# Kernel tuning notes

Hardware: AMD Instinct MI355X
Metric: run time of the kernel (lower is better)

## Reference

```python
import jax, jax.numpy as jnp
import numpy as np

N = 131072
E = 524288
H = 128
EPS = 1e-5

def _layernorm(h, g, b):
    mu = jnp.mean(h, axis=-1, keepdims=True)
    var = jnp.mean((h - mu) ** 2, axis=-1, keepdims=True)
    return (h - mu) * jax.lax.rsqrt(var + EPS) * g + b

def _node_to_node(x, senders, receivers, valid, num_nodes, params):
    # two-way (symmetrized) message passing: gather + scatter_add, then MLP+LN
    W1, b1, W2, b2, W3, b3, g, beta = params
    tws = jnp.concatenate([senders, receivers])
    twr = jnp.concatenate([receivers, senders])
    msg = x[tws]  # [2E', H] gather
    if valid is not None:
        msg = jnp.where(jnp.concatenate([valid, valid])[:, None], msg, 0.0)
    agg = jax.ops.segment_sum(msg, twr, num_segments=num_nodes)  # scatter_add
    h = jax.nn.gelu(agg @ W1 + b1, approximate=False)
    h = jax.nn.gelu(h @ W2 + b2, approximate=False)
    h = h @ W3 + b3
    return _layernorm(h, g, beta)

def setup_inputs() -> dict:
    key = jax.random.key(0)
    ks = jax.random.split(key, 20)
    s = 0.05
    inp = {
        "x": jax.random.normal(ks[0], (N, H), dtype=jnp.float32),
        "edge_index": jax.random.randint(ks[1], (2, E), 0, N, dtype=jnp.int32),
        "pool_p": jax.random.normal(ks[2], (H,), dtype=jnp.float32),
    }
    names = ["dW1", "db1", "dW2", "db2", "dW3", "db3", "dg", "dbeta",
             "uW1", "ub1", "uW2", "ub2", "uW3", "ub3", "ug", "ubeta"]
    shapes = [(H, H), (H,), (H, H), (H,), (H, H), (H,), (H,), (H,),
              (2 * H, H), (H,), (H, H), (H,), (H, H), (H,), (H,), (H,)]
    for i, (nm, sh) in enumerate(zip(names, shapes)):
        if nm in ("dg", "ug"):
            inp[nm] = jnp.ones(sh, dtype=jnp.float32)
        elif nm in ("dbeta", "ubeta") or nm.startswith(("db", "ub")):
            inp[nm] = jnp.zeros(sh, dtype=jnp.float32)
        else:
            inp[nm] = jax.random.normal(ks[3 + i], sh, dtype=jnp.float32) * s
    return inp

def reference(x, edge_index, pool_p,
              dW1, db1, dW2, db2, dW3, db3, dg, dbeta,
              uW1, ub1, uW2, ub2, uW3, ub3, ug, ubeta):
    senders, receivers = edge_index[0], edge_index[1]
    k = N // 2  # TopKPooling ratio=0.5

    # ---- down: TopKPooling ----
    score = x @ pool_p / jnp.linalg.norm(pool_p)  # [N]
    _, perm = jax.lax.top_k(score, k)             # kept node indices
    x_skip = x
    x_p = x[perm] * jnp.tanh(score[perm])[:, None]  # [k, H]
    mask = jnp.zeros((N,), dtype=bool).at[perm].set(True)
    mapping = jnp.zeros((N,), dtype=jnp.int32).at[perm].set(
        jnp.arange(k, dtype=jnp.int32))
    valid = mask[senders] & mask[receivers]
    ps, pr = mapping[senders], mapping[receivers]

    # down conv on pooled graph
    x_d = _node_to_node(x_p, ps, pr, valid, k,
                        (dW1, db1, dW2, db2, dW3, db3, dg, dbeta))

    # ---- up: unpool (indexed scatter write) + skip concat + up conv ----
    recovered = jnp.zeros_like(x_skip).at[perm].set(x_d)
    x_u = jnp.concatenate([recovered, x_skip], axis=-1)  # [N, 2H]
    out = _node_to_node(x_u, senders, receivers, None, N,
                        (uW1, ub1, uW2, ub2, uW3, ub3, ug, ubeta))
    return out
```

## Files before the change

kernel.cpp:

```cpp
#include <hip/hip_runtime.h>

#define N_NODES 131072
#define N_EDGES 524288
#define K_TOP   65536
#define LN_EPS  1e-5f
#define N_TILES (N_NODES / 64)

typedef unsigned int u32;
typedef unsigned short u16;
typedef unsigned long long u64;

typedef __attribute__((ext_vector_type(8))) short bf8;
typedef __attribute__((ext_vector_type(4))) float f4;

#define ST_OFF    0
#define CANON_OFF (64u<<10)
#define PART_OFF  (576u<<10)
#define KEYS_OFF  (1u<<20)
#define TVAL_OFF  (2u<<20)
#define KEPT_OFF  ((2u<<20)+(512u<<10))
#define SBUF_OFF  (3u<<20)
#define OFF_OFF   (35u<<20)
#define ADJ_OFF   (36u<<20)


#define C_DW1 0
#define C_DB1 16384
#define C_DW2 16512
#define C_DB2 32896
#define C_DW3 33024
#define C_DB3 49408
#define C_DG  49536
#define C_DBE 49664
#define C_UW1 49792
#define C_UB1 82560
#define C_UW2 82688
#define C_UB2 99072
#define C_UW3 99200
#define C_UB3 115584
#define C_UG  115712
#define C_UBE 115840
#define C_TOT 115968
#define CT_DW1 115968
#define CT_DW2 132352
#define CT_DW3 148736
#define CT_UW1 165120
#define CT_UW2 197888
#define CT_UW3 214272
#define CT_TOT 230656
#define T_REGION (CT_TOT - CT_DW1)

__device__ __forceinline__ float bflo(u32 u){ return __uint_as_float(u << 16); }
__device__ __forceinline__ float bfhi(u32 u){ return __uint_as_float(u & 0xFFFF0000u); }
__device__ __forceinline__ float bf2f(u16 v){ return __uint_as_float(((u32)v) << 16); }
__device__ __forceinline__ u32 f2bf(float f){
  u32 u = __float_as_uint(f);
  return (u + 0x7FFFu + ((u >> 16) & 1u)) >> 16;
}
__device__ __forceinline__ float gelu_f(float x){
  return 0.5f * x * (1.0f + erff(x * 0.7071067811865476f));
}

__device__ __forceinline__ int swz16(int row, int cc){
  return row * 128 + ((cc ^ (row & 15)) * 8);
}

__device__ __forceinline__ bf8 ld_bf16_chunk(const u32* __restrict__ rowp, int s, int quad){
  uint4 v = *(const uint4*)(rowp + s * 16 + quad * 4);
  return __builtin_bit_cast(bf8, v);
}
__device__ __forceinline__ bf8 scale_bf16_chunk(const u32* __restrict__ rowp, int s, int quad, float tv){
  uint4 v = *(const uint4*)(rowp + s * 16 + quad * 4);
  uint4 q;
  q.x = f2bf(bflo(v.x) * tv) | (f2bf(bfhi(v.x) * tv) << 16);
  q.y = f2bf(bflo(v.y) * tv) | (f2bf(bfhi(v.y) * tv) << 16);
  q.z = f2bf(bflo(v.z) * tv) | (f2bf(bfhi(v.z) * tv) << 16);
  q.w = f2bf(bflo(v.w) * tv) | (f2bf(bfhi(v.w) * tv) << 16);
  return __builtin_bit_cast(bf8, q);
}
__device__ __forceinline__ bf8 cvt_f32_chunk(const float* __restrict__ rowp, int s, int quad, float tv){
  const float* p = rowp + s * 32 + quad * 8;
  float4 f0 = *(const float4*)p;
  float4 f1 = *(const float4*)(p + 4);
  uint4 q;
  q.x = f2bf(f0.x * tv) | (f2bf(f0.y * tv) << 16);
  q.y = f2bf(f0.z * tv) | (f2bf(f0.w * tv) << 16);
  q.z = f2bf(f1.x * tv) | (f2bf(f1.y * tv) << 16);
  q.w = f2bf(f1.z * tv) | (f2bf(f1.w * tv) << 16);
  return __builtin_bit_cast(bf8, q);
}

__device__ __forceinline__ void gemm_ab(const u16* ws, const bf8 a[4], int mn, int quad, f4 acc[8]){
  #pragma unroll
  for (int s = 0; s < 4; s++){
    #pragma unroll
    for (int j = 0; j < 8; j++){
      bf8 b = *(const bf8*)&ws[swz16(j * 16 + mn, s * 4 + quad)];
      acc[j] = __builtin_amdgcn_mfma_f32_16x16x32_bf16(a[s], b, acc[j], 0, 0, 0);
    }
  }
}

struct SelState {
  u64 prefix;
  u32 krem, eqcnt;
  int is_f32;
  u32 pad;
  double inv_norm;
  u32 eqlist[4096];
  u64 eqkey[4096];
};

struct P16 { const void* q[16]; };

__global__ void k_detect(const u32* __restrict__ xw, SelState* st){
  int t = threadIdx.x;
  int cnt = 0;
  for (int i = t; i < 4096; i += 256){
    u32 w = xw[(size_t)i * 2048];
    u32 e = (w >> 23) & 0xFFu;
    if (e >= 97u && e <= 135u) cnt++;
  }
  __shared__ int sh[256];
  sh[t] = cnt; __syncthreads();
  for (int o = 128; o > 0; o >>= 1){ if (t < o) sh[t] += sh[t+o]; __syncthreads(); }
  if (t == 0) st->is_f32 = (sh[0] >= 3072) ? 1 : 0;
}

__global__ void k_init(SelState* st){
  if (threadIdx.x == 0){ st->prefix = 0; st->krem = K_TOP; st->eqcnt = 0; }
}

__global__ void k_canon(P16 ps, const SelState* __restrict__ st, u16* __restrict__ canon){
  const int off[17] = {C_DW1,C_DB1,C_DW2,C_DB2,C_DW3,C_DB3,C_DG,C_DBE,
                       C_UW1,C_UB1,C_UW2,C_UB2,C_UW3,C_UB3,C_UG,C_UBE,C_TOT};
  int i = blockIdx.x * 256 + threadIdx.x;
  if (i >= C_TOT) return;
  int seg = 0;
  #pragma unroll
  for (int s2 = 0; s2 < 16; s2++) if (i >= off[s2+1]) seg = s2 + 1;
  int j = i - off[seg];
  if (st->is_f32) canon[i] = (u16)f2bf(((const float*)ps.q[seg])[j]);
  else            canon[i] = ((const u16*)ps.q[seg])[j];
}

__global__ void k_canon_t(u16* __restrict__ canon){
  const int src[6] = {C_DW1, C_DW2, C_DW3, C_UW1, C_UW2, C_UW3};
  const int dst[7] = {CT_DW1, CT_DW2, CT_DW3, CT_UW1, CT_UW2, CT_UW3, CT_TOT};
  int i = blockIdx.x * 256 + threadIdx.x;
  if (i >= T_REGION) return;
  int g = CT_DW1 + i;
  int seg = 0;
  #pragma unroll
  for (int s2 = 0; s2 < 6; s2++) if (g >= dst[s2+1]) seg = s2 + 1;
  int loc = g - dst[seg];
  int K = (seg == 3) ? 256 : 128;
  int n = loc / K, k = loc % K;
  canon[g] = canon[src[seg] + k * 128 + n];
}

__global__ void k_pnorm(const void* __restrict__ p, SelState* st){
  int t = threadIdx.x;
  float pv = st->is_f32 ? ((const float*)p)[t] : bf2f(((const u16*)p)[t]);
  __shared__ double sh[128];
  sh[t] = (double)pv * (double)pv;
  __syncthreads();
  for (int o = 64; o > 0; o >>= 1){ if (t < o) sh[t] += sh[t+o]; __syncthreads(); }
  if (t == 0) st->inv_norm = 1.0 / sqrt(sh[0]);
}

__global__ __launch_bounds__(256) void k_score(const void* __restrict__ xraw, const void* __restrict__ praw,
                        const SelState* __restrict__ st,
                        u64* __restrict__ keys, float* __restrict__ tval){
  int t = threadIdx.x, lane = t & 63, w = t >> 6;
  int n = blockIdx.x * 4 + w;
  double d;
  if (st->is_f32){
    const float* xf = (const float*)xraw + (size_t)n * 128;
    const float* pf = (const float*)praw;
    d = (double)xf[lane] * (double)pf[lane]
      + (double)xf[64 + lane] * (double)pf[64 + lane];
  } else {
    const u32* xw = (const u32*)xraw + (size_t)n * 64;
    const u32* pw = (const u32*)praw;
    u32 xx = xw[lane], pv = pw[lane];
    d = (double)bflo(xx) * (double)bflo(pv) + (double)bfhi(xx) * (double)bfhi(pv);
  }
  for (int o = 32; o > 0; o >>= 1) d += __shfl_down(d, o, 64);
  if (lane == 0){
    double sc = d * st->inv_norm;
    u64 u = (u64)__double_as_longlong(sc);
    u64 key = (u & 0x8000000000000000ULL) ? ~u : (u | 0x8000000000000000ULL);
    keys[n] = key;
    tval[n] = tanhf((float)sc);
  }
}

__global__ __launch_bounds__(256) void k_histp(const u64* __restrict__ keys,
                                               const SelState* __restrict__ st,
                                               u32* __restrict__ partial, int pass){
  __shared__ u32 h[256];
  int t = threadIdx.x;
  h[t] = 0;
  __syncthreads();
  u64 pref = st->prefix;
  int sh_d = 56 - 8 * pass;
  for (int n = blockIdx.x * 256 + t; n < N_NODES; n += 256 * 256){
    u64 k = keys[n];
    bool m = (pass == 0) ? true : ((k >> (sh_d + 8)) == pref);
    if (m) atomicAdd(&h[(u32)((k >> sh_d) & 255)], 1u);
  }
  __syncthreads();
  partial[blockIdx.x * 256 + t] = h[t];
}

__global__ void k_scanp(const u32* __restrict__ partial, SelState* st){
  __shared__ u32 tot[256];
  int t = threadIdx.x;
  u32 s = 0;
  for (int b = 0; b < 256; b++) s += partial[b * 256 + t];
  tot[t] = s;
  __syncthreads();
  if (t == 0){
    u32 target = st->krem;
    u32 cum = 0; int chosen = 255;
    for (int b = 255; b >= 0; b--){
      if (cum + tot[b] >= target){ chosen = b; break; }
      cum += tot[b];
    }
    st->prefix = (st->prefix << 8) | (u64)(u32)chosen;
    st->krem = target - cum;
  }
}

__global__ void k_mark(const u64* __restrict__ keys, SelState* st, u32* __restrict__ kept){
  int n = blockIdx.x * blockDim.x + threadIdx.x;
  u64 k = keys[n];
  u32 t32 = (u32)(k >> 32);
  u32 T = (u32)st->prefix;
  kept[n] = (t32 > T) ? 1u : 0u;
  if (t32 == T){
    u32 i = atomicAdd(&st->eqcnt, 1u);
    if (i < 4096){ st->eqlist[i] = (u32)n; st->eqkey[i] = k; }
  }
}

__global__ void k_tie(SelState* st, u32* __restrict__ kept){
  u32 m = st->eqcnt; if (m > 4096) m = 4096;
  u32 r = st->krem;
  for (u32 i = threadIdx.x; i < m; i += blockDim.x){
    u64 ki = st->eqkey[i]; u32 ii = st->eqlist[i];
    u32 rank = 0;
    for (u32 j = 0; j < m; j++){
      u64 kj = st->eqkey[j];
      rank += (kj > ki || (kj == ki && st->eqlist[j] < ii)) ? 1u : 0u;
    }
    if (rank < r) kept[ii] = 1u;
  }
}

__global__ __launch_bounds__(256) void k_deg(const int* __restrict__ se, const int* __restrict__ re,
                                             u32* __restrict__ deg){
  int e = blockIdx.x * 256 + threadIdx.x;
  int s = se[e], r = re[e];
  atomicAdd(&deg[s], 1u);
  atomicAdd(&deg[r], 1u);
}

__global__ __launch_bounds__(256) void k_scan1(const u32* __restrict__ deg, u32* __restrict__ bsum){
  __shared__ u32 sh[256];
  int t = threadIdx.x;
  int base = blockIdx.x * 1024 + t * 4;
  u32 s = deg[base] + deg[base+1] + deg[base+2] + deg[base+3];
  sh[t] = s; __syncthreads();
  for (int o = 128; o > 0; o >>= 1){ if (t < o) sh[t] += sh[t+o]; __syncthreads(); }
  if (t == 0) bsum[blockIdx.x] = sh[0];
}

__global__ void k_scan2(u32* __restrict__ bsum){
  __shared__ u32 sh[128];
  int t = threadIdx.x;
  u32 v = bsum[t];
  sh[t] = v; __syncthreads();
  for (int o = 1; o < 128; o <<= 1){
    u32 x = (t >= o) ? sh[t-o] : 0u;
    __syncthreads();
    sh[t] += x;
    __syncthreads();
  }
  bsum[t] = sh[t] - v;
}

__global__ __launch_bounds__(256) void k_scan3(const u32* __restrict__ bsum,
                                               const u32* __restrict__ deg, u32* __restrict__ off){
  __shared__ u32 sh[256];
  int t = threadIdx.x;
  int base = blockIdx.x * 1024 + t * 4;
  u32 v0 = deg[base], v1 = deg[base+1], v2 = deg[base+2], v3 = deg[base+3];
  u32 s = v0 + v1 + v2 + v3;
  sh[t] = s; __syncthreads();
  for (int o = 1; o < 256; o <<= 1){
    u32 x = (t >= o) ? sh[t-o] : 0u;
    __syncthreads();
    sh[t] += x;
    __syncthreads();
  }
  u32 ex = sh[t] - s + bsum[blockIdx.x];
  off[base]   = ex; ex += v0;
  off[base+1] = ex; ex += v1;
  off[base+2] = ex; ex += v2;
  off[base+3] = ex;
  if (blockIdx.x == 0 && t == 0) off[N_NODES] = 2u * N_EDGES;
}

__global__ void k_gcinit(const u32* __restrict__ off, u32* __restrict__ gcur){
  int t = threadIdx.x;
  gcur[t] = off[t * 512];
}

__global__ __launch_bounds__(256) void k_bin(const int* __restrict__ se, const int* __restrict__ re,
                                             u32* __restrict__ gcur, u32* __restrict__ pairs){
  __shared__ u32 cnt[256], sc[256], base[256], cur[256], gpos[256];
  __shared__ u32 stage[8192];
  int t = threadIdx.x;
  cnt[t] = 0;
  __syncthreads();
  int e0 = blockIdx.x * 4096;
  for (int i = t; i < 4096; i += 256){
    int s = se[e0 + i], r = re[e0 + i];
    atomicAdd(&cnt[(u32)r >> 9], 1u);
    atomicAdd(&cnt[(u32)s >> 9], 1u);
  }
  __syncthreads();
  sc[t] = cnt[t];
  __syncthreads();
  for (int o = 1; o < 256; o <<= 1){
    u32 x = (t >= o) ? sc[t - o] : 0u;
    __syncthreads();
    sc[t] += x;
    __syncthreads();
  }
  base[t] = sc[t] - cnt[t];
  cur[t] = base[t];
  gpos[t] = atomicAdd(&gcur[t], cnt[t]);
  __syncthreads();
  for (int i = t; i < 4096; i += 256){
    u32 s = (u32)se[e0 + i], r = (u32)re[e0 + i];
    u32 b1 = r >> 9, p1 = ((r & 511u) << 17) | s;
    u32 b2 = s >> 9, p2 = ((s & 511u) << 17) | r;
    stage[atomicAdd(&cur[b1], 1u)] = p1;
    stage[atomicAdd(&cur[b2], 1u)] = p2;
  }
  __syncthreads();
  int lane = t & 63, wv = t >> 6;
  for (int b = wv; b < 256; b += 4){
    u32 n = cnt[b], src = base[b], dst = gpos[b];
    for (u32 i = lane; i < n; i += 64)
      pairs[dst + i] = stage[src + i];
  }
}

__global__ __launch_bounds__(256) void k_place(const u32* __restrict__ off,
                                               const u32* __restrict__ pairs,
                                               u32* __restrict__ adj){
  __shared__ u32 offl[513];
  __shared__ u32 curl[512];
  int b = blockIdx.x, t = threadIdx.x;
  for (int i = t; i < 513; i += 256) offl[i] = off[b * 512 + i];
  for (int i = t; i < 512; i += 256) curl[i] = 0;
  __syncthreads();
  u32 beg = offl[0], end = offl[512];
  for (u32 i = beg + t; i < end; i += 256){
    u32 p = pairs[i];
    u32 nl = p >> 17, m = p & 0x1FFFFu;
    u32 slot = offl[nl] + atomicAdd(&curl[nl], 1u);
    adj[slot] = m;
  }
}


__global__ __launch_bounds__(256, 3) void k_proj_down(
    const void* __restrict__ xraw, const float* __restrict__ tval,
    const u16* __restrict__ W1T, const SelState* __restrict__ st,
    const u32* __restrict__ kept, u32* __restrict__ S)
{
  __shared__ u16 w1s[128 * 128];
  __shared__ u16 os[64 * 128];
  int t = threadIdx.x, lane = t & 63, wv = t >> 6;
  int m0 = wv * 16, mn = lane & 15, quad = lane >> 4;

  for (int i = t; i < 2048; i += 256){
    int row = i >> 4, cc = i & 15;
    *(uint4*)&w1s[swz16(row, cc)] = *(const uint4*)(W1T + row * 128 + cc * 8);
  }
  int isf = st->is_f32;
  __syncthreads();

  for (int tile = blockIdx.x; tile < N_TILES; tile += gridDim.x){
    int row0 = tile * 64;
    int arow = row0 + m0 + mn;
    float tv = tval[arow];
    bf8 a[4];
    if (isf){
      const float* xf = (const float*)xraw + (size_t)arow * 128;
      #pragma unroll
      for (int s = 0; s < 4; s++) a[s] = cvt_f32_chunk(xf, s, quad, tv);
    } else {
      const u32* xw = (const u32*)xraw + (size_t)arow * 64;
      #pragma unroll
      for (int s = 0; s < 4; s++) a[s] = scale_bf16_chunk(xw, s, quad, tv);
    }
    f4 acc[8];
    #pragma unroll
    for (int j = 0; j < 8; j++){ acc[j][0]=0.f; acc[j][1]=0.f; acc[j][2]=0.f; acc[j][3]=0.f; }
    gemm_ab(w1s, a, mn, quad, acc);

    #pragma unroll
    for (int j = 0; j < 8; j++){
      int c = j * 16 + mn;
      #pragma unroll
      for (int rg = 0; rg < 4; rg++){
        int row = m0 + quad * 4 + rg;
        os[row * 128 + ((c >> 3) ^ (row & 15)) * 8 + (c & 7)] = (u16)f2bf(acc[j][rg]);
      }
    }
    __builtin_amdgcn_wave_barrier();
    int rl = m0 + (lane >> 2), qt = lane & 3;
    u32 kp = kept[row0 + rl];
    u32* out = S + (size_t)(row0 + rl) * 64;
    #pragma unroll
    for (int i = 0; i < 4; i++){
      int cc = qt * 4 + i;
      uint4 w = *(const uint4*)&os[swz16(rl, cc)];
      if (!kp){ w.x = 0; w.y = 0; w.z = 0; w.w = 0; }
      *(uint4*)(out + cc * 4) = w;
    }
    __builtin_amdgcn_wave_barrier();
  }
}

__global__ __launch_bounds__(256, 2) void k_proj_up(
    const u32* __restrict__ R, const void* __restrict__ xraw,
    const u16* __restrict__ W1T, const SelState* __restrict__ st,
    u32* __restrict__ S2)
{
  __shared__ u16 was[128 * 128];
  __shared__ u16 wbs[128 * 128];
  __shared__ u16 os[64 * 128];
  int t = threadIdx.x, lane = t & 63, wv = t >> 6;
  int m0 = wv * 16, mn = lane & 15, quad = lane >> 4;

  for (int i = t; i < 2048; i += 256){
    int row = i >> 4, cc = i & 15;
    *(uint4*)&was[swz16(row, cc)] = *(const uint4*)(W1T + row * 256 + cc * 8);
    *(uint4*)&wbs[swz16(row, cc)] = *(const uint4*)(W1T + row * 256 + 128 + cc * 8);
  }
  int isf = st->is_f32;
  __syncthreads();

  for (int tile = blockIdx.x; tile < N_TILES; tile += gridDim.x){
    int row0 = tile * 64;
    int arow = row0 + m0 + mn;
    bf8 a[4];
    const u32* rp = R + (size_t)arow * 64;
    #pragma unroll
    for (int s = 0; s < 4; s++) a[s] = ld_bf16_chunk(rp, s, quad);
    f4 acc[8];
    #pragma unroll
    for (int j = 0; j < 8; j++){ acc[j][0]=0.f; acc[j][1]=0.f; acc[j][2]=0.f; acc[j][3]=0.f; }
    gemm_ab(was, a, mn, quad, acc);

    if (isf){
      const float* xf = (const float*)xraw + (size_t)arow * 128;
      #pragma unroll
      for (int s = 0; s < 4; s++) a[s] = cvt_f32_chunk(xf, s, quad, 1.0f);
    } else {
      const u32* xw = (const u32*)xraw + (size_t)arow * 64;
      #pragma unroll
      for (int s = 0; s < 4; s++) a[s] = ld_bf16_chunk(xw, s, quad);
    }
    gemm_ab(wbs, a, mn, quad, acc);

    #pragma unroll
    for (int j = 0; j < 8; j++){
      int c = j * 16 + mn;
      #pragma unroll
      for (int rg = 0; rg < 4; rg++){
        int row = m0 + quad * 4 + rg;
        os[row * 128 + ((c >> 3) ^ (row & 15)) * 8 + (c & 7)] = (u16)f2bf(acc[j][rg]);
      }
    }
    __builtin_amdgcn_wave_barrier();
    int rl = m0 + (lane >> 2), qt = lane & 3;
    u32* out = S2 + (size_t)(row0 + rl) * 64;
    #pragma unroll
    for (int i = 0; i < 4; i++){
      int cc = qt * 4 + i;
      *(uint4*)(out + cc * 4) = *(const uint4*)&os[swz16(rl, cc)];
    }
    __builtin_amdgcn_wave_barrier();
  }
}

template<int IS_DOWN>
__global__ __launch_bounds__(256, 4) void k_agg(
    const u32* __restrict__ Smsg, const u32* __restrict__ off, const u32* __restrict__ adj,
    const u16* __restrict__ cb1, const u32* __restrict__ kept,
    u32* __restrict__ H)
{
  int t = threadIdx.x, lane = t & 63, wv = t >> 6;
  float b1l = bf2f(cb1[2 * lane]), b1h = bf2f(cb1[2 * lane + 1]);
  int base = blockIdx.x * 16 + wv * 4;
  #pragma unroll 1
  for (int rr = 0; rr < 4; rr++){
    int n = base + rr;
    if (IS_DOWN && !kept[n]){ H[(size_t)n * 64 + lane] = 0u; continue; }
    u32 jb = off[n], je = off[n + 1];
    float a0 = 0.f, a1 = 0.f;
    u32 j = jb;
    for (; j + 8 <= je; j += 8){
      u32 e0 = adj[j],   e1 = adj[j+1], e2 = adj[j+2], e3 = adj[j+3];
      u32 e4 = adj[j+4], e5 = adj[j+5], e6 = adj[j+6], e7 = adj[j+7];
      u32 w0 = Smsg[(size_t)e0 * 64 + lane];
      u32 w1 = Smsg[(size_t)e1 * 64 + lane];
      u32 w2 = Smsg[(size_t)e2 * 64 + lane];
      u32 w3 = Smsg[(size_t)e3 * 64 + lane];
      u32 w4 = Smsg[(size_t)e4 * 64 + lane];
      u32 w5 = Smsg[(size_t)e5 * 64 + lane];
      u32 w6 = Smsg[(size_t)e6 * 64 + lane];
      u32 w7 = Smsg[(size_t)e7 * 64 + lane];
      a0 += ((bflo(w0) + bflo(w1)) + (bflo(w2) + bflo(w3)))
          + ((bflo(w4) + bflo(w5)) + (bflo(w6) + bflo(w7)));
      a1 += ((bfhi(w0) + bfhi(w1)) + (bfhi(w2) + bfhi(w3)))
          + ((bfhi(w4) + bfhi(w5)) + (bfhi(w6) + bfhi(w7)));
    }
    for (; j + 4 <= je; j += 4){
      u32 e0 = adj[j], e1 = adj[j+1], e2 = adj[j+2], e3 = adj[j+3];
      u32 w0 = Smsg[(size_t)e0 * 64 + lane];
      u32 w1 = Smsg[(size_t)e1 * 64 + lane];
      u32 w2 = Smsg[(size_t)e2 * 64 + lane];
      u32 w3 = Smsg[(size_t)e3 * 64 + lane];
      a0 += (bflo(w0) + bflo(w1)) + (bflo(w2) + bflo(w3));
      a1 += (bfhi(w0) + bfhi(w1)) + (bfhi(w2) + bfhi(w3));
    }
    for (; j < je; j++){
      u32 w = Smsg[(size_t)adj[j] * 64 + lane];
      a0 += bflo(w); a1 += bfhi(w);
    }
    H[(size_t)n * 64 + lane] = f2bf(gelu_f(a0 + b1l)) | (f2bf(gelu_f(a1 + b1h)) << 16);
  }
}

template<int IS_DOWN>
__global__ __launch_bounds__(256, 2) void k_mlp(
    const u32* __restrict__ H,
    const u16* __restrict__ cW2T, const u16* __restrict__ cb2,
    const u16* __restrict__ cW3T, const u16* __restrict__ cb3,
    const u16* __restrict__ cg, const u16* __restrict__ cbe,
    const u32* __restrict__ kept, const SelState* __restrict__ st,
    u32* __restrict__ Rout, void* __restrict__ fout)
{
  __shared__ u16 w2s[128 * 128];
  __shared__ u16 w3s[128 * 128];
  __shared__ u16 os[64 * 128];
  int t = threadIdx.x, lane = t & 63, wv = t >> 6;
  int m0 = wv * 16, mn = lane & 15, quad = lane >> 4;

  for (int i = t; i < 2048; i += 256){
    int row = i >> 4, cc = i & 15;
    *(uint4*)&w2s[swz16(row, cc)] = *(const uint4*)(cW2T + row * 128 + cc * 8);
    *(uint4*)&w3s[swz16(row, cc)] = *(const uint4*)(cW3T + row * 128 + cc * 8);
  }
  float b2v[8], b3v[8], gv[8], bev[8];
  #pragma unroll
  for (int j = 0; j < 8; j++){
    int c = j * 16 + mn;
    b2v[j] = bf2f(cb2[c]); b3v[j] = bf2f(cb3[c]);
    gv[j]  = bf2f(cg[c]);  bev[j] = bf2f(cbe[c]);
  }
  int isf = st->is_f32;
  __syncthreads();

  for (int tile = blockIdx.x; tile < N_TILES; tile += gridDim.x){
    int row0 = tile * 64;
    int arow = row0 + m0 + mn;

    bf8 a[4];
    const u32* hp = H + (size_t)arow * 64;
    #pragma unroll
    for (int s = 0; s < 4; s++) a[s] = ld_bf16_chunk(hp, s, quad);
    f4 acc[8];
    #pragma unroll
    for (int j = 0; j < 8; j++){ acc[j][0]=0.f; acc[j][1]=0.f; acc[j][2]=0.f; acc[j][3]=0.f; }
    gemm_ab(w2s, a, mn, quad, acc);

    #pragma unroll
    for (int j = 0; j < 8; j++){
      int c = j * 16 + mn;
      #pragma unroll
      for (int rg = 0; rg < 4; rg++){
        int row = m0 + quad * 4 + rg;
        os[row * 128 + ((c >> 3) ^ (row & 15)) * 8 + (c & 7)] = (u16)f2bf(gelu_f(acc[j][rg] + b2v[j]));
      }
    }
    __builtin_amdgcn_wave_barrier();

    #pragma unroll
    for (int s = 0; s < 4; s++) a[s] = *(const bf8*)&os[swz16(m0 + mn, s * 4 + quad)];
    #pragma unroll
    for (int j = 0; j < 8; j++){ acc[j][0]=0.f; acc[j][1]=0.f; acc[j][2]=0.f; acc[j][3]=0.f; }
    gemm_ab(w3s, a, mn, quad, acc);

    #pragma unroll
    for (int j = 0; j < 8; j++){
      #pragma unroll
      for (int rg = 0; rg < 4; rg++) acc[j][rg] += b3v[j];
    }
    float s1[4] = {0.f,0.f,0.f,0.f}, s2[4] = {0.f,0.f,0.f,0.f};
    #pragma unroll
    for (int j = 0; j < 8; j++){
      #pragma unroll
      for (int rg = 0; rg < 4; rg++){
        float v = acc[j][rg];
        s1[rg] += v; s2[rg] += v * v;
      }
    }
    #pragma unroll
    for (int o = 1; o < 16; o <<= 1){
      #pragma unroll
      for (int rg = 0; rg < 4; rg++){
        s1[rg] += __shfl_xor(s1[rg], o, 64);
        s2[rg] += __shfl_xor(s2[rg], o, 64);
      }
    }
    float mu[4], rs[4];
    #pragma unroll
    for (int rg = 0; rg < 4; rg++){
      mu[rg] = s1[rg] * 0.0078125f;
      float var = s2[rg] * 0.0078125f - mu[rg] * mu[rg];
      rs[rg] = rsqrtf(var + LN_EPS);
    }
    #pragma unroll
    for (int j = 0; j < 8; j++){
      #pragma unroll
      for (int rg = 0; rg < 4; rg++)
        acc[j][rg] = (acc[j][rg] - mu[rg]) * rs[rg] * gv[j] + bev[j];
    }

    if (!IS_DOWN && isf){
      float* fo = (float*)fout;
      #pragma unroll
      for (int j = 0; j < 8; j++){
        #pragma unroll
        for (int rg = 0; rg < 4; rg++)
          fo[(size_t)(row0 + m0 + quad * 4 + rg) * 128 + j * 16 + mn] = acc[j][rg];
      }
      continue;
    }

    __builtin_amdgcn_wave_barrier();
    #pragma unroll
    for (int j = 0; j < 8; j++){
      int c = j * 16 + mn;
      #pragma unroll
      for (int rg = 0; rg < 4; rg++){
        int row = m0 + quad * 4 + rg;
        os[row * 128 + ((c >> 3) ^ (row & 15)) * 8 + (c & 7)] = (u16)f2bf(acc[j][rg]);
      }
    }
    __builtin_amdgcn_wave_barrier();
    int rl = m0 + (lane >> 2), qt = lane & 3;
    u32 kp = IS_DOWN ? kept[row0 + rl] : 1u;
    u32* out = (IS_DOWN ? Rout : (u32*)fout) + (size_t)(row0 + rl) * 64;
    #pragma unroll
    for (int i = 0; i < 4; i++){
      int cc = qt * 4 + i;
      uint4 w = *(const uint4*)&os[swz16(rl, cc)];
      if (!kp){ w.x = 0; w.y = 0; w.z = 0; w.w = 0; }
      *(uint4*)(out + cc * 4) = w;
    }
    __builtin_amdgcn_wave_barrier();
  }
}


extern "C" void kernel_launch(void* const* d_in, const int* in_sizes, int n_in,
                              void* d_out, int out_size, void* d_ws, size_t ws_size,
                              hipStream_t stream)
{
  const void* x     = d_in[0];
  const int* eidx   = (const int*)d_in[1];
  const void* poolp = d_in[2];
  const int* senders = eidx;
  const int* receivers = eidx + N_EDGES;

  char* ws = (char*)d_ws;
  SelState* st = (SelState*)(ws + ST_OFF);
  u16*  canon  = (u16*) (ws + CANON_OFF);
  u32*  partial= (u32*) (ws + PART_OFF);
  u64*  keys   = (u64*) (ws + KEYS_OFF);
  float* tval  = (float*)(ws + TVAL_OFF);
  u32*  kept   = (u32*) (ws + KEPT_OFF);
  u32*  Sbuf   = (u32*) (ws + SBUF_OFF);
  u32*  off    = (u32*) (ws + OFF_OFF);
  u32*  adj    = (u32*) (ws + ADJ_OFF);
  u32*  deg    = (u32*) (ws + KEYS_OFF);
  u32*  bsum   = partial;
  u32*  gcur   = partial + 512;
  u32*  pairs  = Sbuf;
  u32*  Dbuf   = (u32*) d_out;

  P16 ps;
  for (int i = 0; i < 16; i++) ps.q[i] = d_in[3 + i];

  k_detect<<<1, 256, 0, stream>>>((const u32*)x, st);
  k_init<<<1, 64, 0, stream>>>(st);
  k_canon<<<(C_TOT + 255) / 256, 256, 0, stream>>>(ps, st, canon);
  k_canon_t<<<(T_REGION + 255) / 256, 256, 0, stream>>>(canon);
  k_pnorm<<<1, 128, 0, stream>>>(poolp, st);
  k_score<<<N_NODES / 4, 256, 0, stream>>>(x, poolp, st, keys, tval);
  for (int pass = 0; pass < 4; pass++){
    k_histp<<<256, 256, 0, stream>>>(keys, st, partial, pass);
    k_scanp<<<1, 256, 0, stream>>>(partial, st);
  }
  k_mark<<<N_NODES / 256, 256, 0, stream>>>(keys, st, kept);
  k_tie<<<1, 256, 0, stream>>>(st, kept);

  hipMemsetAsync(deg, 0, (size_t)N_NODES * 4, stream);
  k_deg<<<N_EDGES / 256, 256, 0, stream>>>(senders, receivers, deg);
  k_scan1<<<128, 256, 0, stream>>>(deg, bsum);
  k_scan2<<<1, 128, 0, stream>>>(bsum);
  k_scan3<<<128, 256, 0, stream>>>(bsum, deg, off);
  k_gcinit<<<1, 256, 0, stream>>>(off, gcur);
  k_bin<<<N_EDGES / 4096, 256, 0, stream>>>(senders, receivers, gcur, pairs);
  k_place<<<256, 256, 0, stream>>>(off, pairs, adj);

  k_proj_down<<<768, 256, 0, stream>>>(x, tval, canon + CT_DW1, st, kept, Sbuf);
  k_agg<1><<<N_NODES / 16, 256, 0, stream>>>(Sbuf, off, adj, canon + C_DB1, kept, Dbuf);
  k_mlp<1><<<512, 256, 0, stream>>>(Dbuf,
      canon + CT_DW2, canon + C_DB2, canon + CT_DW3, canon + C_DB3,
      canon + C_DG, canon + C_DBE, kept, st, Sbuf, nullptr);

  k_proj_up<<<512, 256, 0, stream>>>(Sbuf, x, canon + CT_UW1, st, Dbuf);
  k_agg<0><<<N_NODES / 16, 256, 0, stream>>>(Dbuf, off, adj, canon + C_UB1, kept, Sbuf);
  k_mlp<0><<<512, 256, 0, stream>>>(Sbuf,
      canon + CT_UW2, canon + C_UB2, canon + CT_UW3, canon + C_UB3,
      canon + C_UG, canon + C_UBE, kept, st, nullptr, d_out);
}
```

Before: 525.1 us.

## Merge small setup kernels and mask dropped senders in down aggregation

Folds state init into k_detect, merges the weight canonicalization and transpose kernels into one, and computes the pool-vector norm inside k_score. It also zeroes degrees in k_mark instead of a memset, and initializes gcur and a zero row inside k_scan3. These changes cut about five kernel launches and a memset. In the down aggregation, messages from non-kept senders are redirected to a zero row, which adds a per-edge kept lookup. This may be a correctness fix if the projected buffer holds garbage for dropped nodes.

```diff
diff --git a/kernel.cpp b/kernel.cpp
--- a/kernel.cpp
+++ b/kernel.cpp
@@ -20,6 +20,7 @@
 #define TVAL_OFF  (2u<<20)
 #define KEPT_OFF  ((2u<<20)+(512u<<10))
 #define SBUF_OFF  (3u<<20)
+#define DEG_OFF   (34u<<20)
 #define OFF_OFF   (35u<<20)
 #define ADJ_OFF   (36u<<20)
 
@@ -48,7 +49,6 @@
 #define CT_UW2 197888
 #define CT_UW3 214272
 #define CT_TOT 230656
-#define T_REGION (CT_TOT - CT_DW1)
 
 __device__ __forceinline__ float bflo(u32 u){ return __uint_as_float(u << 16); }
 __device__ __forceinline__ float bfhi(u32 u){ return __uint_as_float(u & 0xFFFF0000u); }
@@ -59,6 +59,9 @@
 }
 __device__ __forceinline__ float gelu_f(float x){
   return 0.5f * x * (1.0f + erff(x * 0.7071067811865476f));
+}
+__device__ __forceinline__ float2 f2add(float2 a, float2 b){
+  return make_float2(a.x + b.x, a.y + b.y);
 }
 
 __device__ __forceinline__ int swz16(int row, int cc){
@@ -124,49 +127,39 @@
   __shared__ int sh[256];
   sh[t] = cnt; __syncthreads();
   for (int o = 128; o > 0; o >>= 1){ if (t < o) sh[t] += sh[t+o]; __syncthreads(); }
-  if (t == 0) st->is_f32 = (sh[0] >= 3072) ? 1 : 0;
-}
-
-__global__ void k_init(SelState* st){
-  if (threadIdx.x == 0){ st->prefix = 0; st->krem = K_TOP; st->eqcnt = 0; }
+  if (t == 0){
+    st->is_f32 = (sh[0] >= 3072) ? 1 : 0;
+    st->prefix = 0; st->krem = K_TOP; st->eqcnt = 0;
+  }
 }
 
 __global__ void k_canon(P16 ps, const SelState* __restrict__ st, u16* __restrict__ canon){
-  const int off[17] = {C_DW1,C_DB1,C_DW2,C_DB2,C_DW3,C_DB3,C_DG,C_DBE,
-                       C_UW1,C_UB1,C_UW2,C_UB2,C_UW3,C_UB3,C_UG,C_UBE,C_TOT};
   int i = blockIdx.x * 256 + threadIdx.x;
-  if (i >= C_TOT) return;
-  int seg = 0;
-  #pragma unroll
-  for (int s2 = 0; s2 < 16; s2++) if (i >= off[s2+1]) seg = s2 + 1;
-  int j = i - off[seg];
-  if (st->is_f32) canon[i] = (u16)f2bf(((const float*)ps.q[seg])[j]);
-  else            canon[i] = ((const u16*)ps.q[seg])[j];
-}
-
-__global__ void k_canon_t(u16* __restrict__ canon){
-  const int src[6] = {C_DW1, C_DW2, C_DW3, C_UW1, C_UW2, C_UW3};
-  const int dst[7] = {CT_DW1, CT_DW2, CT_DW3, CT_UW1, CT_UW2, CT_UW3, CT_TOT};
-  int i = blockIdx.x * 256 + threadIdx.x;
-  if (i >= T_REGION) return;
-  int g = CT_DW1 + i;
-  int seg = 0;
-  #pragma unroll
-  for (int s2 = 0; s2 < 6; s2++) if (g >= dst[s2+1]) seg = s2 + 1;
-  int loc = g - dst[seg];
-  int K = (seg == 3) ? 256 : 128;
-  int n = loc / K, k = loc % K;
-  canon[g] = canon[src[seg] + k * 128 + n];
-}
-
-__global__ void k_pnorm(const void* __restrict__ p, SelState* st){
-  int t = threadIdx.x;
-  float pv = st->is_f32 ? ((const float*)p)[t] : bf2f(((const u16*)p)[t]);
-  __shared__ double sh[128];
-  sh[t] = (double)pv * (double)pv;
-  __syncthreads();
-  for (int o = 64; o > 0; o >>= 1){ if (t < o) sh[t] += sh[t+o]; __syncthreads(); }
-  if (t == 0) st->inv_norm = 1.0 / sqrt(sh[0]);
+  if (i >= CT_TOT) return;
+  int isf = st->is_f32;
+  if (i < C_TOT){
+    const int off[17] = {C_DW1,C_DB1,C_DW2,C_DB2,C_DW3,C_DB3,C_DG,C_DBE,
+                         C_UW1,C_UB1,C_UW2,C_UB2,C_UW3,C_UB3,C_UG,C_UBE,C_TOT};
+    int seg = 0;
+    #pragma unroll
+    for (int s2 = 0; s2 < 16; s2++) if (i >= off[s2+1]) seg = s2 + 1;
+    int j = i - off[seg];
+    if (isf) canon[i] = (u16)f2bf(((const float*)ps.q[seg])[j]);
+    else     canon[i] = ((const u16*)ps.q[seg])[j];
+  } else {
+    const int dst[7] = {CT_DW1, CT_DW2, CT_DW3, CT_UW1, CT_UW2, CT_UW3, CT_TOT};
+    const int wq[6]  = {0, 2, 4, 8, 10, 12};
+    int g = i;
+    int seg = 0;
+    #pragma unroll
+    for (int s2 = 0; s2 < 6; s2++) if (g >= dst[s2+1]) seg = s2 + 1;
+    int loc = g - dst[seg];
+    int K = (seg == 3) ? 256 : 128;
+    int n = loc / K, k = loc % K;
+    int src = k * 128 + n;
+    if (isf) canon[g] = (u16)f2bf(((const float*)ps.q[wq[seg]])[src]);
+    else     canon[g] = ((const u16*)ps.q[wq[seg]])[src];
+  }
 }
 
 __global__ __launch_bounds__(256) void k_score(const void* __restrict__ xraw, const void* __restrict__ praw,
@@ -174,21 +167,27 @@
                         u64* __restrict__ keys, float* __restrict__ tval){
   int t = threadIdx.x, lane = t & 63, w = t >> 6;
   int n = blockIdx.x * 4 + w;
-  double d;
+  double d, ps;
   if (st->is_f32){
     const float* xf = (const float*)xraw + (size_t)n * 128;
     const float* pf = (const float*)praw;
-    d = (double)xf[lane] * (double)pf[lane]
-      + (double)xf[64 + lane] * (double)pf[64 + lane];
+    double p0 = (double)pf[lane], p1 = (double)pf[64 + lane];
+    d  = (double)xf[lane] * p0 + (double)xf[64 + lane] * p1;
+    ps = p0 * p0 + p1 * p1;
   } else {
     const u32* xw = (const u32*)xraw + (size_t)n * 64;
     const u32* pw = (const u32*)praw;
     u32 xx = xw[lane], pv = pw[lane];
-    d = (double)bflo(xx) * (double)bflo(pv) + (double)bfhi(xx) * (double)bfhi(pv);
-  }
-  for (int o = 32; o > 0; o >>= 1) d += __shfl_down(d, o, 64);
+    double p0 = (double)bflo(pv), p1 = (double)bfhi(pv);
+    d  = (double)bflo(xx) * p0 + (double)bfhi(xx) * p1;
+    ps = p0 * p0 + p1 * p1;
+  }
+  for (int o = 32; o > 0; o >>= 1){
+    d  += __shfl_down(d,  o, 64);
+    ps += __shfl_down(ps, o, 64);
+  }
   if (lane == 0){
-    double sc = d * st->inv_norm;
+    double sc = d * (1.0 / sqrt(ps));
     u64 u = (u64)__double_as_longlong(sc);
     u64 key = (u & 0x8000000000000000ULL) ? ~u : (u | 0x8000000000000000ULL);
     keys[n] = key;
@@ -233,12 +232,14 @@
   }
 }
 
-__global__ void k_mark(const u64* __restrict__ keys, SelState* st, u32* __restrict__ kept){
+__global__ void k_mark(const u64* __restrict__ keys, SelState* st, u32* __restrict__ kept,
+                       u32* __restrict__ deg){
   int n = blockIdx.x * blockDim.x + threadIdx.x;
   u64 k = keys[n];
   u32 t32 = (u32)(k >> 32);
   u32 T = (u32)st->prefix;
   kept[n] = (t32 > T) ? 1u : 0u;
+  deg[n] = 0u;
   if (t32 == T){
     u32 i = atomicAdd(&st->eqcnt, 1u);
     if (i < 4096){ st->eqlist[i] = (u32)n; st->eqkey[i] = k; }
@@ -292,7 +293,8 @@
 }
 
 __global__ __launch_bounds__(256) void k_scan3(const u32* __restrict__ bsum,
-                                               const u32* __restrict__ deg, u32* __restrict__ off){
+                                               const u32* __restrict__ deg, u32* __restrict__ off,
+                                               u32* __restrict__ gcur, u32* __restrict__ zrow){
   __shared__ u32 sh[256];
   int t = threadIdx.x;
   int base = blockIdx.x * 1024 + t * 4;
@@ -306,16 +308,15 @@
     __syncthreads();
   }
   u32 ex = sh[t] - s + bsum[blockIdx.x];
+  if ((t & 127) == 0) gcur[base >> 9] = ex;
   off[base]   = ex; ex += v0;
   off[base+1] = ex; ex += v1;
   off[base+2] = ex; ex += v2;
   off[base+3] = ex;
-  if (blockIdx.x == 0 && t == 0) off[N_NODES] = 2u * N_EDGES;
-}
-
-__global__ void k_gcinit(const u32* __restrict__ off, u32* __restrict__ gcur){
-  int t = threadIdx.x;
-  gcur[t] = off[t * 512];
+  if (blockIdx.x == 0){
+    if (t == 0) off[N_NODES] = 2u * N_EDGES;
+    if (t < 64) zrow[t] = 0u;
+  }
 }
 
 __global__ __launch_bounds__(256) void k_bin(const int* __restrict__ se, const int* __restrict__ re,
@@ -503,10 +504,19 @@
 }
 
 template<int IS_DOWN>
+__device__ __forceinline__ const u32* rowsel(const u32* __restrict__ Smsg, u32 e,
+                                             const u32* __restrict__ kept,
+                                             const u32* __restrict__ zrow){
+  const u32* p = Smsg + (size_t)e * 64;
+  if (IS_DOWN) p = kept[e] ? p : zrow;
+  return p;
+}
+
+template<int IS_DOWN>
 __global__ __launch_bounds__(256, 4) void k_agg(
     const u32* __restrict__ Smsg, const u32* __restrict__ off, const u32* __restrict__ adj,
     const u16* __restrict__ cb1, const u32* __restrict__ kept,
-    u32* __restrict__ H)
+    const u32* __restrict__ zrow, u32* __restrict__ H)
 {
   int t = threadIdx.x, lane = t & 63, wv = t >> 6;
   float b1l = bf2f(cb1[2 * lane]), b1h = bf2f(cb1[2 * lane + 1]);
@@ -516,38 +526,48 @@
     int n = base + rr;
     if (IS_DOWN && !kept[n]){ H[(size_t)n * 64 + lane] = 0u; continue; }
     u32 jb = off[n], je = off[n + 1];
-    float a0 = 0.f, a1 = 0.f;
+    float2 a = make_float2(0.f, 0.f);
     u32 j = jb;
     for (; j + 8 <= je; j += 8){
-      u32 e0 = adj[j],   e1 = adj[j+1], e2 = adj[j+2], e3 = adj[j+3];
-      u32 e4 = adj[j+4], e5 = adj[j+5], e6 = adj[j+6], e7 = adj[j+7];
-      u32 w0 = Smsg[(size_t)e0 * 64 + lane];
-      u32 w1 = Smsg[(size_t)e1 * 64 + lane];
-      u32 w2 = Smsg[(size_t)e2 * 64 + lane];
-      u32 w3 = Smsg[(size_t)e3 * 64 + lane];
-      u32 w4 = Smsg[(size_t)e4 * 64 + lane];
-      u32 w5 = Smsg[(size_t)e5 * 64 + lane];
-      u32 w6 = Smsg[(size_t)e6 * 64 + lane];
-      u32 w7 = Smsg[(size_t)e7 * 64 + lane];
-      a0 += ((bflo(w0) + bflo(w1)) + (bflo(w2) + bflo(w3)))
-          + ((bflo(w4) + bflo(w5)) + (bflo(w6) + bflo(w7)));
-      a1 += ((bfhi(w0) + bfhi(w1)) + (bfhi(w2) + bfhi(w3)))
-          + ((bfhi(w4) + bfhi(w5)) + (bfhi(w6) + bfhi(w7)));
+      const u32* r0 = rowsel<IS_DOWN>(Smsg, adj[j],   kept, zrow);
+      const u32* r1 = rowsel<IS_DOWN>(Smsg, adj[j+1], kept, zrow);
+      const u32* r2 = rowsel<IS_DOWN>(Smsg, adj[j+2], kept, zrow);
+      const u32* r3 = rowsel<IS_DOWN>(Smsg, adj[j+3], kept, zrow);
+      const u32* r4 = rowsel<IS_DOWN>(Smsg, adj[j+4], kept, zrow);
+      const u32* r5 = rowsel<IS_DOWN>(Smsg, adj[j+5], kept, zrow);
+      const u32* r6 = rowsel<IS_DOWN>(Smsg, adj[j+6], kept, zrow);
+      const u32* r7 = rowsel<IS_DOWN>(Smsg, adj[j+7], kept, zrow);
+      u32 w0 = r0[lane], w1 = r1[lane], w2 = r2[lane], w3 = r3[lane];
+      u32 w4 = r4[lane], w5 = r5[lane], w6 = r6[lane], w7 = r7[lane];
+      float2 v0 = make_float2(bflo(w0), bfhi(w0));
+      float2 v1 = make_float2(bflo(w1), bfhi(w1));
+      float2 v2 = make_float2(bflo(w2), bfhi(w2));
+      float2 v3 = make_float2(bflo(w3), bfhi(w3));
+      float2 v4 = make_float2(bflo(w4), bfhi(w4));
+      float2 v5 = make_float2(bflo(w5), bfhi(w5));
+      float2 v6 = make_float2(bflo(w6), bfhi(w6));
+      float2 v7 = make_float2(bflo(w7), bfhi(w7));
+      a = f2add(a, f2add(f2add(f2add(v0, v1), f2add(v2, v3)),
+                         f2add(f2add(v4, v5), f2add(v6, v7))));
     }
     for (; j + 4 <= je; j += 4){
-      u32 e0 = adj[j], e1 = adj[j+1], e2 = adj[j+2], e3 = adj[j+3];
-      u32 w0 = Smsg[(size_t)e0 * 64 + lane];
-      u32 w1 = Smsg[(size_t)e1 * 64 + lane];
-      u32 w2 = Smsg[(size_t)e2 * 64 + lane];
-      u32 w3 = Smsg[(size_t)e3 * 64 + lane];
-      a0 += (bflo(w0) + bflo(w1)) + (bflo(w2) + bflo(w3));
-      a1 += (bfhi(w0) + bfhi(w1)) + (bfhi(w2) + bfhi(w3));
+      const u32* r0 = rowsel<IS_DOWN>(Smsg, adj[j],   kept, zrow);
+      const u32* r1 = rowsel<IS_DOWN>(Smsg, adj[j+1], kept, zrow);
+      const u32* r2 = rowsel<IS_DOWN>(Smsg, adj[j+2], kept, zrow);
+      const u32* r3 = rowsel<IS_DOWN>(Smsg, adj[j+3], kept, zrow);
+      u32 w0 = r0[lane], w1 = r1[lane], w2 = r2[lane], w3 = r3[lane];
+      float2 v0 = make_float2(bflo(w0), bfhi(w0));
+      float2 v1 = make_float2(bflo(w1), bfhi(w1));
+      float2 v2 = make_float2(bflo(w2), bfhi(w2));
+      float2 v3 = make_float2(bflo(w3), bfhi(w3));
+      a = f2add(a, f2add(f2add(v0, v1), f2add(v2, v3)));
     }
     for (; j < je; j++){
-      u32 w = Smsg[(size_t)adj[j] * 64 + lane];
-      a0 += bflo(w); a1 += bfhi(w);
-    }
-    H[(size_t)n * 64 + lane] = f2bf(gelu_f(a0 + b1l)) | (f2bf(gelu_f(a1 + b1h)) << 16);
+      const u32* r0 = rowsel<IS_DOWN>(Smsg, adj[j], kept, zrow);
+      u32 w = r0[lane];
+      a = f2add(a, make_float2(bflo(w), bfhi(w)));
+    }
+    H[(size_t)n * 64 + lane] = f2bf(gelu_f(a.x + b1l)) | (f2bf(gelu_f(a.y + b1h)) << 16);
   }
 }
 
@@ -702,11 +722,12 @@
   float* tval  = (float*)(ws + TVAL_OFF);
   u32*  kept   = (u32*) (ws + KEPT_OFF);
   u32*  Sbuf   = (u32*) (ws + SBUF_OFF);
+  u32*  deg    = (u32*) (ws + DEG_OFF);
   u32*  off    = (u32*) (ws + OFF_OFF);
   u32*  adj    = (u32*) (ws + ADJ_OFF);
-  u32*  deg    = (u32*) (ws + KEYS_OFF);
   u32*  bsum   = partial;
   u32*  gcur   = partial + 512;
+  u32*  zrow   = partial + 2048;
   u32*  pairs  = Sbuf;
   u32*  Dbuf   = (u32*) d_out;
 
@@ -714,35 +735,30 @@
   for (int i = 0; i < 16; i++) ps.q[i] = d_in[3 + i];
 
   k_detect<<<1, 256, 0, stream>>>((const u32*)x, st);
-  k_init<<<1, 64, 0, stream>>>(st);
-  k_canon<<<(C_TOT + 255) / 256, 256, 0, stream>>>(ps, st, canon);
-  k_canon_t<<<(T_REGION + 255) / 256, 256, 0, stream>>>(canon);
-  k_pnorm<<<1, 128, 0, stream>>>(poolp, st);
+  k_canon<<<(CT_TOT + 255) / 256, 256, 0, stream>>>(ps, st, canon);
   k_score<<<N_NODES / 4, 256, 0, stream>>>(x, poolp, st, keys, tval);
   for (int pass = 0; pass < 4; pass++){
     k_histp<<<256, 256, 0, stream>>>(keys, st, partial, pass);
     k_scanp<<<1, 256, 0, stream>>>(partial, st);
   }
-  k_mark<<<N_NODES / 256, 256, 0, stream>>>(keys, st, kept);
+  k_mark<<<N_NODES / 256, 256, 0, stream>>>(keys, st, kept, deg);
   k_tie<<<1, 256, 0, stream>>>(st, kept);
 
-  hipMemsetAsync(deg, 0, (size_t)N_NODES * 4, stream);
   k_deg<<<N_EDGES / 256, 256, 0, stream>>>(senders, receivers, deg);
   k_scan1<<<128, 256, 0, stream>>>(deg, bsum);
   k_scan2<<<1, 128, 0, stream>>>(bsum);
-  k_scan3<<<128, 256, 0, stream>>>(bsum, deg, off);
-  k_gcinit<<<1, 256, 0, stream>>>(off, gcur);
+  k_scan3<<<128, 256, 0, stream>>>(bsum, deg, off, gcur, zrow);
   k_bin<<<N_EDGES / 4096, 256, 0, stream>>>(senders, receivers, gcur, pairs);
   k_place<<<256, 256, 0, stream>>>(off, pairs, adj);
 
   k_proj_down<<<768, 256, 0, stream>>>(x, tval, canon + CT_DW1, st, kept, Sbuf);
-  k_agg<1><<<N_NODES / 16, 256, 0, stream>>>(Sbuf, off, adj, canon + C_DB1, kept, Dbuf);
+  k_agg<1><<<N_NODES / 16, 256, 0, stream>>>(Sbuf, off, adj, canon + C_DB1, kept, zrow, Dbuf);
   k_mlp<1><<<512, 256, 0, stream>>>(Dbuf,
       canon + CT_DW2, canon + C_DB2, canon + CT_DW3, canon + C_DB3,
       canon + C_DG, canon + C_DBE, kept, st, Sbuf, nullptr);
 
   k_proj_up<<<512, 256, 0, stream>>>(Sbuf, x, canon + CT_UW1, st, Dbuf);
-  k_agg<0><<<N_NODES / 16, 256, 0, stream>>>(Dbuf, off, adj, canon + C_UB1, kept, Sbuf);
+  k_agg<0><<<N_NODES / 16, 256, 0, stream>>>(Dbuf, off, adj, canon + C_UB1, kept, zrow, Sbuf);
   k_mlp<0><<<512, 256, 0, stream>>>(Sbuf,
       canon + CT_UW2, canon + C_UB2, canon + CT_UW3, canon + C_UB3,
       canon + C_UG, canon + C_UBE, kept, st, nullptr, d_out);
```

After: 528.6 us. No clear change (+0.7%).
